# Performance work log

Measured on AMD Instinct MI355X. Metric: run time of the kernel, lower is better.

## Reference

```python
import jax, jax.numpy as jnp
import numpy as np

D_MODEL = 1024
NUM_HEADS = 16
D_K = D_MODEL // NUM_HEADS
NEG = -10000.0


def setup_inputs() -> dict:
    key = jax.random.key(0)
    ks = jax.random.split(key, 8)
    B, S = 2, 2048
    query = jax.random.normal(ks[0], (B, S, D_MODEL), dtype=jnp.float32)
    key_t = jax.random.normal(ks[1], (B, S, D_MODEL), dtype=jnp.float32)
    value = jax.random.normal(ks[2], (B, S, D_MODEL), dtype=jnp.float32)
    mask = jax.random.randint(ks[3], (B, S), 0, 2, dtype=jnp.int32)
    scale = 1.0 / np.sqrt(D_MODEL)
    Wq = jax.random.normal(ks[4], (D_MODEL, D_MODEL), dtype=jnp.float32) * scale
    Wk = jax.random.normal(ks[5], (D_MODEL, D_MODEL), dtype=jnp.float32) * scale
    Wv = jax.random.normal(ks[6], (D_MODEL, D_MODEL), dtype=jnp.float32) * scale
    Wo = jax.random.normal(ks[7], (D_MODEL, D_MODEL), dtype=jnp.float32) * scale
    return {"query": query, "key": key_t, "value": value, "mask": mask,
            "Wq": Wq, "Wk": Wk, "Wv": Wv, "Wo": Wo}


def reference(query, key, value, mask, Wq, Wk, Wv, Wo):
    B, Sq, _ = query.shape
    Sk = key.shape[1]
    # Linear projections (torch Linear: x @ W.T), split heads -> [B,H,S,d_k]
    def proj(x, W, S):
        return (x @ W.T).reshape(B, S, NUM_HEADS, D_K).transpose(0, 2, 1, 3)
    Q = proj(query, Wq, Sq)
    K = proj(key, Wk, Sk)
    V = proj(value, Wv, Sk)
    # scores [B,H,Sq,Sk]
    scores = jnp.einsum("bhqd,bhkd->bhqk", Q, K) / jnp.sqrt(jnp.float32(D_K))
    # padding mask [B,Sk] -> [B,1,1,Sk]
    pad = mask[:, None, None, :]
    scores = jnp.where(pad == 0, NEG, scores)
    # causal mask (mask_future=True)
    causal = jnp.tril(jnp.ones((Sq, Sk), dtype=bool))
    scores = jnp.where(causal, scores, NEG)
    probs = jax.nn.softmax(scores, axis=-1)  # dropout p=0.0 -> identity
    out = jnp.einsum("bhqk,bhkd->bhqd", probs, V)
    out = out.transpose(0, 2, 1, 3).reshape(B, Sq, D_MODEL)
    return out @ Wo.T
```

## Files before the change

### kernel.cpp

```cpp
#include <hip/hip_runtime.h>
#include <hip/hip_bf16.h>

typedef __attribute__((ext_vector_type(8))) short s16x8;
typedef __attribute__((ext_vector_type(4))) float f32x4;

#define MFMA16(a,b,c) __builtin_amdgcn_mfma_f32_16x16x32_bf16((a),(b),(c),0,0,0)

#define GLD16(gp, lp) __builtin_amdgcn_global_load_lds( \
  (const __attribute__((address_space(1))) unsigned int*)(gp), \
  (__attribute__((address_space(3))) unsigned int*)(lp), 16, 0, 0)

static __device__ __forceinline__ unsigned short f2bu(float f) {
  __hip_bfloat16 h = __float2bfloat16(f);
  unsigned short u; __builtin_memcpy(&u, &h, 2); return u;
}
static __device__ __forceinline__ float b2f(unsigned short u) {
  unsigned int x = ((unsigned int)u) << 16; float f; __builtin_memcpy(&f, &x, 4); return f;
}

__global__ __launch_bounds__(256) void cast_all(const float* __restrict__ q, const float* __restrict__ k,
                                                const float* __restrict__ v,
                                                const float* __restrict__ Wq, const float* __restrict__ Wk,
                                                const float* __restrict__ Wv, const float* __restrict__ Wo,
                                                unsigned short* __restrict__ qc, unsigned short* __restrict__ kc,
                                                unsigned short* __restrict__ vc,
                                                unsigned short* __restrict__ wq, unsigned short* __restrict__ wk,
                                                unsigned short* __restrict__ wv, unsigned short* __restrict__ wo) {
  const int y = blockIdx.y;
  const float* in; unsigned short* out; int n4;
  switch (y) {
    case 0: in = q;  out = qc; n4 = 1048576; break;
    case 1: in = k;  out = kc; n4 = 1048576; break;
    case 2: in = v;  out = vc; n4 = 1048576; break;
    case 3: in = Wq; out = wq; n4 = 262144; break;
    case 4: in = Wk; out = wk; n4 = 262144; break;
    case 5: in = Wv; out = wv; n4 = 262144; break;
    default: in = Wo; out = wo; n4 = 262144; break;
  }
  int i = blockIdx.x * 256 + threadIdx.x;
  if (i < n4) {
    float4 val = *(const float4*)(in + (size_t)i * 4);
    unsigned int p0 = (unsigned int)f2bu(val.x) | ((unsigned int)f2bu(val.y) << 16);
    unsigned int p1 = (unsigned int)f2bu(val.z) | ((unsigned int)f2bu(val.w) << 16);
    uint2 pk; pk.x = p0; pk.y = p1;
    *(uint2*)(out + (size_t)i * 4) = pk;
  }
}

static __device__ __forceinline__ void gemm_core(const unsigned short* __restrict__ Aw,
                                                 const unsigned short* __restrict__ Bw,
                                                 int m0, int n0,
                                                 f32x4 (&acc)[4][4],
                                                 unsigned short (*As)[64], unsigned short (*Bs)[64]) {
  const int K = 1024;
  const int tid = threadIdx.x;
  const int lane = tid & 63, wave = tid >> 6;
  const int wm = wave >> 1, wn = wave & 1;
  const int row16 = lane & 15, kgrp = lane >> 4;
  const int srow = lane >> 3, sslot = (lane & 7) ^ srow;
  const int sw = row16 & 7;

  for (int k0 = 0; k0 < K; k0 += 64) {
#pragma unroll
    for (int i = 0; i < 4; i++) {
      int rr = (wave * 4 + i) * 8 + srow;
      GLD16(Aw + (size_t)(m0 + rr) * K + k0 + sslot * 8, (char*)As + (wave * 4 + i) * 1024);
      GLD16(Bw + (size_t)(n0 + rr) * K + k0 + sslot * 8, (char*)Bs + (wave * 4 + i) * 1024);
    }
    __syncthreads();

#pragma unroll
    for (int kk = 0; kk < 2; kk++) {
      s16x8 af[4], bfr[4];
#pragma unroll
      for (int mi = 0; mi < 4; mi++) {
        int rr = wm * 64 + mi * 16 + row16;
        af[mi] = *(const s16x8*)((char*)&As[rr][0] + ((kk * 4 + kgrp) ^ sw) * 16);
      }
#pragma unroll
      for (int ni = 0; ni < 4; ni++) {
        int rr = wn * 64 + ni * 16 + row16;
        bfr[ni] = *(const s16x8*)((char*)&Bs[rr][0] + ((kk * 4 + kgrp) ^ sw) * 16);
      }
#pragma unroll
      for (int mi = 0; mi < 4; mi++)
#pragma unroll
        for (int ni = 0; ni < 4; ni++)
          acc[mi][ni] = MFMA16(af[mi], bfr[ni], acc[mi][ni]);
    }
    __syncthreads();
  }
}

__global__ __launch_bounds__(256) void qkv_gemm(const unsigned short* __restrict__ qc,
                                                const unsigned short* __restrict__ kc,
                                                const unsigned short* __restrict__ vc,
                                                const unsigned short* __restrict__ Wqb,
                                                const unsigned short* __restrict__ Wkb,
                                                const unsigned short* __restrict__ Wvb,
                                                unsigned short* __restrict__ Qb,
                                                unsigned short* __restrict__ Kb,
                                                unsigned short* __restrict__ Vt) {
  __shared__ unsigned short As[128][64];
  __shared__ unsigned short Bs[128][64];
  const int xcd = blockIdx.x & 7, u = blockIdx.x >> 3;
  const int g = xcd * 12 + (u >> 3);
  const int z = g >> 5, mstrip = g & 31;
  const int m0 = mstrip * 128, n0 = (u & 7) * 128;

  const unsigned short* A = (z == 0) ? qc : (z == 1) ? kc : vc;
  const unsigned short* Bw = (z == 0) ? Wqb : (z == 1) ? Wkb : Wvb;

  f32x4 acc[4][4] = {};
  gemm_core(A, Bw, m0, n0, acc, As, Bs);

  const int lane = threadIdx.x & 63, wave = threadIdx.x >> 6;
  const int wm = wave >> 1, wn = wave & 1;
  const int row16 = lane & 15, kgrp = lane >> 4;

  if (z < 2) {
    unsigned short* C = z ? Kb : Qb;
#pragma unroll
    for (int mi = 0; mi < 4; mi++)
#pragma unroll
      for (int ni = 0; ni < 4; ni++)
#pragma unroll
        for (int r = 0; r < 4; r++) {
          int row = m0 + wm * 64 + mi * 16 + kgrp * 4 + r;
          int col = n0 + wn * 64 + ni * 16 + row16;
          C[(size_t)row * 1024 + col] = f2bu(acc[mi][ni][r]);
        }
  } else {
#pragma unroll
    for (int mi = 0; mi < 4; mi++)
#pragma unroll
      for (int ni = 0; ni < 4; ni++) {
        int mb = m0 + wm * 64 + mi * 16 + kgrp * 4;
        int col = n0 + wn * 64 + ni * 16 + row16;
        int bb = mb >> 11, s = mb & 2047;
        unsigned int p0 = (unsigned int)f2bu(acc[mi][ni][0]) | ((unsigned int)f2bu(acc[mi][ni][1]) << 16);
        unsigned int p1 = (unsigned int)f2bu(acc[mi][ni][2]) | ((unsigned int)f2bu(acc[mi][ni][3]) << 16);
        uint2 pk; pk.x = p0; pk.y = p1;
        *(uint2*)&Vt[(((size_t)(bb * 1024 + col)) << 11) + s] = pk;
      }
  }
}

__global__ __launch_bounds__(256) void gemm_wo(const unsigned short* __restrict__ A,
                                               const unsigned short* __restrict__ Bw,
                                               float* __restrict__ C) {
  __shared__ unsigned short As[128][64];
  __shared__ unsigned short Bs[128][64];
  const int xcd = blockIdx.x & 7, u = blockIdx.x >> 3;
  const int g = xcd * 4 + (u >> 3);
  const int m0 = g * 128, n0 = (u & 7) * 128;

  f32x4 acc[4][4] = {};
  gemm_core(A, Bw, m0, n0, acc, As, Bs);

  const int lane = threadIdx.x & 63, wave = threadIdx.x >> 6;
  const int wm = wave >> 1, wn = wave & 1;
  const int row16 = lane & 15, kgrp = lane >> 4;
#pragma unroll
  for (int mi = 0; mi < 4; mi++)
#pragma unroll
    for (int ni = 0; ni < 4; ni++)
#pragma unroll
      for (int r = 0; r < 4; r++) {
        int row = m0 + wm * 64 + mi * 16 + kgrp * 4 + r;
        int col = n0 + wn * 64 + ni * 16 + row16;
        C[(size_t)row * 1024 + col] = acc[mi][ni][r];
      }
}

__global__ __launch_bounds__(256) void fu_kernel(const int* __restrict__ mask, int* __restrict__ fu) {
  const int S = 2048;
  int b = blockIdx.x;
  __shared__ int red[256];
  int best = S;
  for (int k = threadIdx.x; k < S; k += 256)
    if (mask[b * S + k] != 0 && k < best) best = k;
  red[threadIdx.x] = best;
  __syncthreads();
  for (int s = 128; s > 0; s >>= 1) {
    if (threadIdx.x < s) red[threadIdx.x] = min(red[threadIdx.x], red[threadIdx.x + s]);
    __syncthreads();
  }
  if (threadIdx.x == 0) fu[b] = red[0];
}

__global__ __launch_bounds__(256) void reduce_vt(const unsigned short* __restrict__ Vt,
                                                 float* __restrict__ vsum) {
  __shared__ float red[256];
  const unsigned short* p = Vt + ((size_t)blockIdx.x << 11) + threadIdx.x * 8;
  uint4 u = *(const uint4*)p;
  float s = b2f((unsigned short)(u.x & 0xffff));
  s += b2f((unsigned short)(u.x >> 16));
  s += b2f((unsigned short)(u.y & 0xffff));
  s += b2f((unsigned short)(u.y >> 16));
  s += b2f((unsigned short)(u.z & 0xffff));
  s += b2f((unsigned short)(u.z >> 16));
  s += b2f((unsigned short)(u.w & 0xffff));
  s += b2f((unsigned short)(u.w >> 16));
  red[threadIdx.x] = s;
  __syncthreads();
  for (int st = 128; st > 0; st >>= 1) {
    if (threadIdx.x < st) red[threadIdx.x] += red[threadIdx.x + st];
    __syncthreads();
  }
  if (threadIdx.x == 0) vsum[blockIdx.x] = red[0];
}

__global__ __launch_bounds__(256) void flash_attn4(const unsigned short* __restrict__ Q,
                                                   const unsigned short* __restrict__ Kp,
                                                   const unsigned short* __restrict__ Vt,
                                                   const int* __restrict__ mask,
                                                   const int* __restrict__ fu,
                                                   const float* __restrict__ vsum,
                                                   unsigned short* __restrict__ O) {
  const int S = 2048, DM = 1024;
  const int xcd = blockIdx.x & 7, idx = blockIdx.x >> 3;
  const int bh = xcd * 4 + (idx >> 4);
  const int pairq = idx & 15;
  const int b = bh >> 4, h = bh & 15;
  const int tid = threadIdx.x, lane = tid & 63, wave = tid >> 6;
  const int row16 = lane & 15, kgrp = lane >> 4;

  __shared__ unsigned short Ks[2][64][64];
  __shared__ unsigned short Vs[2][64][64];
  __shared__ unsigned short Ps[4][16][72];

  const size_t base = ((size_t)b * S) * DM + h * 64;
  const size_t vtb = ((size_t)(b * 1024 + h * 64)) * S;
  const int* maskb = mask + b * S;

  const int srow = lane >> 3;
  const int sslot = (lane & 7) ^ srow;

  const int fub = fu[b];
  const float* vs = vsum + b * DM + h * 64;
  const int sw = row16 & 7;

#pragma unroll
  for (int pass = 0; pass < 2; ++pass) {
    const int qt = pass ? (31 - pairq) : pairq;
    const int q0 = qt * 64 + wave * 16;
    const int qg = q0 + row16;
    const int nt = qt + 1;

    s16x8 qf0 = *(const s16x8*)&Q[base + (size_t)qg * DM + kgrp * 8];
    s16x8 qf1 = *(const s16x8*)&Q[base + (size_t)qg * DM + 32 + kgrp * 8];

    f32x4 oacc[4] = {};
    float m_run = -1e30f, l_run = 0.f;

    auto stage = [&](int t, int bf) {
      const int kb = t * 64;
#pragma unroll
      for (int c2 = 0; c2 < 2; c2++) {
        const int r = wave * 16 + c2 * 8 + srow;
        GLD16(Kp + base + (size_t)(kb + r) * DM + sslot * 8,
              (char*)&Ks[bf][0][0] + (wave * 2 + c2) * 1024);
        GLD16(Vt + vtb + (size_t)r * S + kb + sslot * 8,
              (char*)&Vs[bf][0][0] + (wave * 2 + c2) * 1024);
      }
    };

    stage(0, 0);
    asm volatile("s_waitcnt vmcnt(0)" ::: "memory");
    __syncthreads();

    int cur = 0;
    for (int t = 0; t < nt; ++t) {
      if (t + 1 < nt) stage(t + 1, cur ^ 1);
      const int kb = t * 64;

      f32x4 sc[4];
#pragma unroll
      for (int nf = 0; nf < 4; nf++) {
        const int rr = nf * 16 + row16;
        s16x8 k0 = *(const s16x8*)&Ks[cur][rr][(kgrp ^ sw) * 8];
        s16x8 k1 = *(const s16x8*)&Ks[cur][rr][((4 + kgrp) ^ sw) * 8];
        f32x4 a = {};
        a = MFMA16(k0, qf0, a);
        a = MFMA16(k1, qf1, a);
        sc[nf] = a;
      }

#pragma unroll
      for (int nf = 0; nf < 4; nf++) {
        const int kbase = kb + nf * 16 + kgrp * 4;
        int4 mv = *(const int4*)&maskb[kbase];
#pragma unroll
        for (int r = 0; r < 4; r++) {
          int m_ok = (r == 0) ? mv.x : (r == 1) ? mv.y : (r == 2) ? mv.z : mv.w;
          float s = sc[nf][r] * 0.125f;
          sc[nf][r] = (kbase + r > qg || m_ok == 0) ? -10000.0f : s;
        }
      }

      float t01 = fmaxf(fmaxf(sc[0][0], sc[0][1]), fmaxf(sc[0][2], sc[0][3]));
      float t23 = fmaxf(fmaxf(sc[1][0], sc[1][1]), fmaxf(sc[1][2], sc[1][3]));
      float t45 = fmaxf(fmaxf(sc[2][0], sc[2][1]), fmaxf(sc[2][2], sc[2][3]));
      float t67 = fmaxf(fmaxf(sc[3][0], sc[3][1]), fmaxf(sc[3][2], sc[3][3]));
      float tmax = fmaxf(fmaxf(t01, t23), fmaxf(t45, t67));
      tmax = fmaxf(tmax, __shfl_xor(tmax, 16));
      tmax = fmaxf(tmax, __shfl_xor(tmax, 32));

      float mnew = fmaxf(m_run, tmax);
      float alpha = __expf(m_run - mnew);
      m_run = mnew;

      float rsum = 0.f;
#pragma unroll
      for (int nf = 0; nf < 4; nf++)
#pragma unroll
        for (int r = 0; r < 4; r++) {
          float p = __expf(sc[nf][r] - mnew);
          sc[nf][r] = p;
          rsum += p;
        }
      rsum += __shfl_xor(rsum, 16);
      rsum += __shfl_xor(rsum, 32);
      l_run = l_run * alpha + rsum;
#pragma unroll
      for (int nf2 = 0; nf2 < 4; nf2++)
#pragma unroll
        for (int r = 0; r < 4; r++) oacc[nf2][r] *= alpha;

#pragma unroll
      for (int nf = 0; nf < 4; nf++) {
        uint2 pk;
        pk.x = (unsigned int)f2bu(sc[nf][0]) | ((unsigned int)f2bu(sc[nf][1]) << 16);
        pk.y = (unsigned int)f2bu(sc[nf][2]) | ((unsigned int)f2bu(sc[nf][3]) << 16);
        *(uint2*)&Ps[wave][row16][nf * 16 + kgrp * 4] = pk;
      }
      s16x8 pf0 = *(const s16x8*)&Ps[wave][row16][kgrp * 8];
      s16x8 pf1 = *(const s16x8*)&Ps[wave][row16][32 + kgrp * 8];

#pragma unroll
      for (int nf2 = 0; nf2 < 4; nf2++) {
        const int rr = nf2 * 16 + row16;
        s16x8 v0 = *(const s16x8*)&Vs[cur][rr][(kgrp ^ sw) * 8];
        s16x8 v1 = *(const s16x8*)&Vs[cur][rr][((4 + kgrp) ^ sw) * 8];
        oacc[nf2] = MFMA16(v0, pf0, oacc[nf2]);
        oacc[nf2] = MFMA16(v1, pf1, oacc[nf2]);
      }

      asm volatile("s_waitcnt vmcnt(0)" ::: "memory");
      __syncthreads();
      cur ^= 1;
    }

    const float rl = 1.0f / l_run;
#pragma unroll
    for (int nf2 = 0; nf2 < 4; nf2++) {
      const int d0 = nf2 * 16 + kgrp * 4;
      float v0 = oacc[nf2][0] * rl, v1 = oacc[nf2][1] * rl;
      float v2 = oacc[nf2][2] * rl, v3 = oacc[nf2][3] * rl;
      if (qg < fub) {
        float4 vv = *(const float4*)&vs[d0];
        v0 = vv.x * (1.0f / 2048.0f);
        v1 = vv.y * (1.0f / 2048.0f);
        v2 = vv.z * (1.0f / 2048.0f);
        v3 = vv.w * (1.0f / 2048.0f);
      }
      uint2 pk;
      pk.x = (unsigned int)f2bu(v0) | ((unsigned int)f2bu(v1) << 16);
      pk.y = (unsigned int)f2bu(v2) | ((unsigned int)f2bu(v3) << 16);
      *(uint2*)&O[base + (size_t)qg * DM + d0] = pk;
    }
  }
}

extern "C" void kernel_launch(void* const* d_in, const int* in_sizes, int n_in,
                              void* d_out, int out_size, void* d_ws, size_t ws_size,
                              hipStream_t stream) {
  const float* q    = (const float*)d_in[0];
  const float* k    = (const float*)d_in[1];
  const float* v    = (const float*)d_in[2];
  const int*   mask = (const int*)d_in[3];
  const float* Wq   = (const float*)d_in[4];
  const float* Wk   = (const float*)d_in[5];
  const float* Wv   = (const float*)d_in[6];
  const float* Wo   = (const float*)d_in[7];
  float* out = (float*)d_out;
  char* ws = (char*)d_ws;

  unsigned short* Wqb  = (unsigned short*)(ws + (size_t)0);
  unsigned short* Wkb  = (unsigned short*)(ws + ((size_t)2 << 20));
  unsigned short* Wvb  = (unsigned short*)(ws + ((size_t)4 << 20));
  unsigned short* Wob  = (unsigned short*)(ws + ((size_t)6 << 20));
  unsigned short* vc   = (unsigned short*)(ws + ((size_t)8 << 20));
  unsigned short* attn = (unsigned short*)(ws + ((size_t)8 << 20));
  unsigned short* Qb   = (unsigned short*)(ws + ((size_t)16 << 20));
  unsigned short* Kb   = (unsigned short*)(ws + ((size_t)24 << 20));
  unsigned short* Vt   = (unsigned short*)(ws + ((size_t)32 << 20));
  float* vsum          = (float*)(ws + ((size_t)40 << 20));
  int*   fub           = (int*)(ws + ((size_t)40 << 20) + (64 << 10));
  unsigned short* qc   = (unsigned short*)d_out;
  unsigned short* kc   = (unsigned short*)d_out + 4194304;

  cast_all<<<dim3(4096, 7), 256, 0, stream>>>(q, k, v, Wq, Wk, Wv, Wo,
                                              qc, kc, vc, Wqb, Wkb, Wvb, Wob);

  qkv_gemm<<<768, 256, 0, stream>>>(qc, kc, vc, Wqb, Wkb, Wvb, Qb, Kb, Vt);

  fu_kernel<<<2, 256, 0, stream>>>(mask, fub);
  reduce_vt<<<2048, 256, 0, stream>>>(Vt, vsum);

  flash_attn4<<<512, 256, 0, stream>>>(Qb, Kb, Vt, mask, fub, vsum, attn);

  gemm_wo<<<256, 256, 0, stream>>>(attn, Wob, out);
}
```

Measured before the change: 151.2 us.

## Split attention into one q-tile per block with additive mask and lazy rescale

The attention kernel no longer pairs two query tiles per block. It launches 1024 blocks, one query tile each, ordered longest-first, and drops the XCD-aware mapping. The padding mask is precomputed as an additive penalty array folded into a single fma with a log2e-prescaled softmax using exp2. The causal compare is applied only on the diagonal tile, and the online-softmax rescale is skipped when no row max increases. This trades per-element ALU work and the paired-tile structure for more blocks and relies on the scheduler to balance the uneven tile lengths. Masked scores now use -30000, which changes the masked value but should not affect the softmax.

New measurement: 144.8 us. 4.2% less time.

```diff
diff --git a/kernel.cpp b/kernel.cpp
--- a/kernel.cpp
+++ b/kernel.cpp
@@ -1,5 +1,6 @@
 #include <hip/hip_runtime.h>
 #include <hip/hip_bf16.h>
+#include <math.h>
 
 typedef __attribute__((ext_vector_type(8))) short s16x8;
 typedef __attribute__((ext_vector_type(4))) float f32x4;
@@ -173,13 +174,17 @@
       }
 }
 
-__global__ __launch_bounds__(256) void fu_kernel(const int* __restrict__ mask, int* __restrict__ fu) {
+__global__ __launch_bounds__(256) void fu_pen_kernel(const int* __restrict__ mask, int* __restrict__ fu,
+                                                     float* __restrict__ pen) {
   const int S = 2048;
   int b = blockIdx.x;
   __shared__ int red[256];
   int best = S;
-  for (int k = threadIdx.x; k < S; k += 256)
-    if (mask[b * S + k] != 0 && k < best) best = k;
+  for (int k = threadIdx.x; k < S; k += 256) {
+    int mv = mask[b * S + k];
+    pen[b * S + k] = mv ? 0.0f : -30000.0f;
+    if (mv != 0 && k < best) best = k;
+  }
   red[threadIdx.x] = best;
   __syncthreads();
   for (int s = 128; s > 0; s >>= 1) {
@@ -211,17 +216,18 @@
   if (threadIdx.x == 0) vsum[blockIdx.x] = red[0];
 }
 
-__global__ __launch_bounds__(256) void flash_attn4(const unsigned short* __restrict__ Q,
+__global__ __launch_bounds__(256) void flash_attn5(const unsigned short* __restrict__ Q,
                                                    const unsigned short* __restrict__ Kp,
                                                    const unsigned short* __restrict__ Vt,
-                                                   const int* __restrict__ mask,
+                                                   const float* __restrict__ pen,
                                                    const int* __restrict__ fu,
                                                    const float* __restrict__ vsum,
                                                    unsigned short* __restrict__ O) {
   const int S = 2048, DM = 1024;
-  const int xcd = blockIdx.x & 7, idx = blockIdx.x >> 3;
-  const int bh = xcd * 4 + (idx >> 4);
-  const int pairq = idx & 15;
+  const float SCALE2 = 0.125f * 1.4426950408889634f;
+  const int bid = blockIdx.x;
+  const int qt = 31 - (bid >> 5);
+  const int bh = bid & 31;
   const int b = bh >> 4, h = bh & 15;
   const int tid = threadIdx.x, lane = tid & 63, wave = tid >> 6;
   const int row16 = lane & 15, kgrp = lane >> 4;
@@ -232,144 +238,152 @@
 
   const size_t base = ((size_t)b * S) * DM + h * 64;
   const size_t vtb = ((size_t)(b * 1024 + h * 64)) * S;
-  const int* maskb = mask + b * S;
+  const float* penb = pen + b * S;
 
   const int srow = lane >> 3;
   const int sslot = (lane & 7) ^ srow;
+  const int sw = row16 & 7;
+
+  const int q0 = qt * 64 + wave * 16;
+  const int qg = q0 + row16;
+  const int nt = qt + 1;
+
+  s16x8 qf0 = *(const s16x8*)&Q[base + (size_t)qg * DM + kgrp * 8];
+  s16x8 qf1 = *(const s16x8*)&Q[base + (size_t)qg * DM + 32 + kgrp * 8];
+
+  f32x4 oacc[4] = {};
+  float m_run = -1e30f, l_run = 0.f;
+
+  auto stage = [&](int t, int bf) {
+    const int kb = t * 64;
+#pragma unroll
+    for (int c2 = 0; c2 < 2; c2++) {
+      const int r = wave * 16 + c2 * 8 + srow;
+      GLD16(Kp + base + (size_t)(kb + r) * DM + sslot * 8,
+            (char*)&Ks[bf][0][0] + (wave * 2 + c2) * 1024);
+      GLD16(Vt + vtb + (size_t)r * S + kb + sslot * 8,
+            (char*)&Vs[bf][0][0] + (wave * 2 + c2) * 1024);
+    }
+  };
+
+  stage(0, 0);
+  asm volatile("s_waitcnt vmcnt(0)" ::: "memory");
+  __syncthreads();
+
+  int cur = 0;
+  for (int t = 0; t < nt; ++t) {
+    if (t + 1 < nt) stage(t + 1, cur ^ 1);
+    const int kb = t * 64;
+
+    float4 pv[4];
+#pragma unroll
+    for (int nf = 0; nf < 4; nf++)
+      pv[nf] = *(const float4*)&penb[kb + nf * 16 + kgrp * 4];
+
+    f32x4 sc[4];
+#pragma unroll
+    for (int nf = 0; nf < 4; nf++) {
+      const int rr = nf * 16 + row16;
+      s16x8 k0 = *(const s16x8*)&Ks[cur][rr][(kgrp ^ sw) * 8];
+      s16x8 k1 = *(const s16x8*)&Ks[cur][rr][((4 + kgrp) ^ sw) * 8];
+      f32x4 a = {};
+      a = MFMA16(k0, qf0, a);
+      a = MFMA16(k1, qf1, a);
+      sc[nf] = a;
+    }
+
+#pragma unroll
+    for (int nf = 0; nf < 4; nf++) {
+      sc[nf][0] = fmaf(sc[nf][0], SCALE2, pv[nf].x);
+      sc[nf][1] = fmaf(sc[nf][1], SCALE2, pv[nf].y);
+      sc[nf][2] = fmaf(sc[nf][2], SCALE2, pv[nf].z);
+      sc[nf][3] = fmaf(sc[nf][3], SCALE2, pv[nf].w);
+    }
+    if (t == nt - 1) {
+#pragma unroll
+      for (int nf = 0; nf < 4; nf++) {
+        const int kbase = kb + nf * 16 + kgrp * 4;
+#pragma unroll
+        for (int r = 0; r < 4; r++)
+          if (kbase + r > qg) sc[nf][r] = -30000.0f;
+      }
+    }
+
+    float t01 = fmaxf(fmaxf(sc[0][0], sc[0][1]), fmaxf(sc[0][2], sc[0][3]));
+    float t23 = fmaxf(fmaxf(sc[1][0], sc[1][1]), fmaxf(sc[1][2], sc[1][3]));
+    float t45 = fmaxf(fmaxf(sc[2][0], sc[2][1]), fmaxf(sc[2][2], sc[2][3]));
+    float t67 = fmaxf(fmaxf(sc[3][0], sc[3][1]), fmaxf(sc[3][2], sc[3][3]));
+    float tmax = fmaxf(fmaxf(t01, t23), fmaxf(t45, t67));
+    tmax = fmaxf(tmax, __shfl_xor(tmax, 16));
+    tmax = fmaxf(tmax, __shfl_xor(tmax, 32));
+
+    if (__any(tmax > m_run)) {
+      float mnew = fmaxf(m_run, tmax);
+      float alpha = __builtin_exp2f(m_run - mnew);
+      m_run = mnew;
+      l_run *= alpha;
+#pragma unroll
+      for (int nf2 = 0; nf2 < 4; nf2++)
+#pragma unroll
+        for (int r = 0; r < 4; r++) oacc[nf2][r] *= alpha;
+    }
+
+    float rsum = 0.f;
+#pragma unroll
+    for (int nf = 0; nf < 4; nf++)
+#pragma unroll
+      for (int r = 0; r < 4; r++) {
+        float p = __builtin_exp2f(sc[nf][r] - m_run);
+        sc[nf][r] = p;
+        rsum += p;
+      }
+    rsum += __shfl_xor(rsum, 16);
+    rsum += __shfl_xor(rsum, 32);
+    l_run += rsum;
+
+#pragma unroll
+    for (int nf = 0; nf < 4; nf++) {
+      uint2 pk;
+      pk.x = (unsigned int)f2bu(sc[nf][0]) | ((unsigned int)f2bu(sc[nf][1]) << 16);
+      pk.y = (unsigned int)f2bu(sc[nf][2]) | ((unsigned int)f2bu(sc[nf][3]) << 16);
+      *(uint2*)&Ps[wave][row16][nf * 16 + kgrp * 4] = pk;
+    }
+    s16x8 pf0 = *(const s16x8*)&Ps[wave][row16][kgrp * 8];
+    s16x8 pf1 = *(const s16x8*)&Ps[wave][row16][32 + kgrp * 8];
+
+#pragma unroll
+    for (int nf2 = 0; nf2 < 4; nf2++) {
+      const int rr = nf2 * 16 + row16;
+      s16x8 v0 = *(const s16x8*)&Vs[cur][rr][(kgrp ^ sw) * 8];
+      s16x8 v1 = *(const s16x8*)&Vs[cur][rr][((4 + kgrp) ^ sw) * 8];
+      oacc[nf2] = MFMA16(v0, pf0, oacc[nf2]);
+      oacc[nf2] = MFMA16(v1, pf1, oacc[nf2]);
+    }
+
+    asm volatile("s_waitcnt vmcnt(0)" ::: "memory");
+    __syncthreads();
+    cur ^= 1;
+  }
 
   const int fub = fu[b];
   const float* vs = vsum + b * DM + h * 64;
-  const int sw = row16 & 7;
-
-#pragma unroll
-  for (int pass = 0; pass < 2; ++pass) {
-    const int qt = pass ? (31 - pairq) : pairq;
-    const int q0 = qt * 64 + wave * 16;
-    const int qg = q0 + row16;
-    const int nt = qt + 1;
-
-    s16x8 qf0 = *(const s16x8*)&Q[base + (size_t)qg * DM + kgrp * 8];
-    s16x8 qf1 = *(const s16x8*)&Q[base + (size_t)qg * DM + 32 + kgrp * 8];
-
-    f32x4 oacc[4] = {};
-    float m_run = -1e30f, l_run = 0.f;
-
-    auto stage = [&](int t, int bf) {
-      const int kb = t * 64;
-#pragma unroll
-      for (int c2 = 0; c2 < 2; c2++) {
-        const int r = wave * 16 + c2 * 8 + srow;
-        GLD16(Kp + base + (size_t)(kb + r) * DM + sslot * 8,
-              (char*)&Ks[bf][0][0] + (wave * 2 + c2) * 1024);
-        GLD16(Vt + vtb + (size_t)r * S + kb + sslot * 8,
-              (char*)&Vs[bf][0][0] + (wave * 2 + c2) * 1024);
-      }
-    };
-
-    stage(0, 0);
-    asm volatile("s_waitcnt vmcnt(0)" ::: "memory");
-    __syncthreads();
-
-    int cur = 0;
-    for (int t = 0; t < nt; ++t) {
-      if (t + 1 < nt) stage(t + 1, cur ^ 1);
-      const int kb = t * 64;
-
-      f32x4 sc[4];
-#pragma unroll
-      for (int nf = 0; nf < 4; nf++) {
-        const int rr = nf * 16 + row16;
-        s16x8 k0 = *(const s16x8*)&Ks[cur][rr][(kgrp ^ sw) * 8];
-        s16x8 k1 = *(const s16x8*)&Ks[cur][rr][((4 + kgrp) ^ sw) * 8];
-        f32x4 a = {};
-        a = MFMA16(k0, qf0, a);
-        a = MFMA16(k1, qf1, a);
-        sc[nf] = a;
-      }
-
-#pragma unroll
-      for (int nf = 0; nf < 4; nf++) {
-        const int kbase = kb + nf * 16 + kgrp * 4;
-        int4 mv = *(const int4*)&maskb[kbase];
-#pragma unroll
-        for (int r = 0; r < 4; r++) {
-          int m_ok = (r == 0) ? mv.x : (r == 1) ? mv.y : (r == 2) ? mv.z : mv.w;
-          float s = sc[nf][r] * 0.125f;
-          sc[nf][r] = (kbase + r > qg || m_ok == 0) ? -10000.0f : s;
-        }
-      }
-
-      float t01 = fmaxf(fmaxf(sc[0][0], sc[0][1]), fmaxf(sc[0][2], sc[0][3]));
-      float t23 = fmaxf(fmaxf(sc[1][0], sc[1][1]), fmaxf(sc[1][2], sc[1][3]));
-      float t45 = fmaxf(fmaxf(sc[2][0], sc[2][1]), fmaxf(sc[2][2], sc[2][3]));
-      float t67 = fmaxf(fmaxf(sc[3][0], sc[3][1]), fmaxf(sc[3][2], sc[3][3]));
-      float tmax = fmaxf(fmaxf(t01, t23), fmaxf(t45, t67));
-      tmax = fmaxf(tmax, __shfl_xor(tmax, 16));
-      tmax = fmaxf(tmax, __shfl_xor(tmax, 32));
-
-      float mnew = fmaxf(m_run, tmax);
-      float alpha = __expf(m_run - mnew);
-      m_run = mnew;
-
-      float rsum = 0.f;
-#pragma unroll
-      for (int nf = 0; nf < 4; nf++)
-#pragma unroll
-        for (int r = 0; r < 4; r++) {
-          float p = __expf(sc[nf][r] - mnew);
-          sc[nf][r] = p;
-          rsum += p;
-        }
-      rsum += __shfl_xor(rsum, 16);
-      rsum += __shfl_xor(rsum, 32);
-      l_run = l_run * alpha + rsum;
-#pragma unroll
-      for (int nf2 = 0; nf2 < 4; nf2++)
-#pragma unroll
-        for (int r = 0; r < 4; r++) oacc[nf2][r] *= alpha;
-
-#pragma unroll
-      for (int nf = 0; nf < 4; nf++) {
-        uint2 pk;
-        pk.x = (unsigned int)f2bu(sc[nf][0]) | ((unsigned int)f2bu(sc[nf][1]) << 16);
-        pk.y = (unsigned int)f2bu(sc[nf][2]) | ((unsigned int)f2bu(sc[nf][3]) << 16);
-        *(uint2*)&Ps[wave][row16][nf * 16 + kgrp * 4] = pk;
-      }
-      s16x8 pf0 = *(const s16x8*)&Ps[wave][row16][kgrp * 8];
-      s16x8 pf1 = *(const s16x8*)&Ps[wave][row16][32 + kgrp * 8];
-
-#pragma unroll
-      for (int nf2 = 0; nf2 < 4; nf2++) {
-        const int rr = nf2 * 16 + row16;
-        s16x8 v0 = *(const s16x8*)&Vs[cur][rr][(kgrp ^ sw) * 8];
-        s16x8 v1 = *(const s16x8*)&Vs[cur][rr][((4 + kgrp) ^ sw) * 8];
-        oacc[nf2] = MFMA16(v0, pf0, oacc[nf2]);
-        oacc[nf2] = MFMA16(v1, pf1, oacc[nf2]);
-      }
-
-      asm volatile("s_waitcnt vmcnt(0)" ::: "memory");
-      __syncthreads();
-      cur ^= 1;
-    }
-
-    const float rl = 1.0f / l_run;
-#pragma unroll
-    for (int nf2 = 0; nf2 < 4; nf2++) {
-      const int d0 = nf2 * 16 + kgrp * 4;
-      float v0 = oacc[nf2][0] * rl, v1 = oacc[nf2][1] * rl;
-      float v2 = oacc[nf2][2] * rl, v3 = oacc[nf2][3] * rl;
-      if (qg < fub) {
-        float4 vv = *(const float4*)&vs[d0];
-        v0 = vv.x * (1.0f / 2048.0f);
-        v1 = vv.y * (1.0f / 2048.0f);
-        v2 = vv.z * (1.0f / 2048.0f);
-        v3 = vv.w * (1.0f / 2048.0f);
-      }
-      uint2 pk;
-      pk.x = (unsigned int)f2bu(v0) | ((unsigned int)f2bu(v1) << 16);
-      pk.y = (unsigned int)f2bu(v2) | ((unsigned int)f2bu(v3) << 16);
-      *(uint2*)&O[base + (size_t)qg * DM + d0] = pk;
-    }
+  const float rl = 1.0f / l_run;
+#pragma unroll
+  for (int nf2 = 0; nf2 < 4; nf2++) {
+    const int d0 = nf2 * 16 + kgrp * 4;
+    float v0 = oacc[nf2][0] * rl, v1 = oacc[nf2][1] * rl;
+    float v2 = oacc[nf2][2] * rl, v3 = oacc[nf2][3] * rl;
+    if (qg < fub) {
+      float4 vv = *(const float4*)&vs[d0];
+      v0 = vv.x * (1.0f / 2048.0f);
+      v1 = vv.y * (1.0f / 2048.0f);
+      v2 = vv.z * (1.0f / 2048.0f);
+      v3 = vv.w * (1.0f / 2048.0f);
+    }
+    uint2 pk;
+    pk.x = (unsigned int)f2bu(v0) | ((unsigned int)f2bu(v1) << 16);
+    pk.y = (unsigned int)f2bu(v2) | ((unsigned int)f2bu(v3) << 16);
+    *(uint2*)&O[base + (size_t)qg * DM + d0] = pk;
   }
 }
 
@@ -398,6 +412,7 @@
   unsigned short* Vt   = (unsigned short*)(ws + ((size_t)32 << 20));
   float* vsum          = (float*)(ws + ((size_t)40 << 20));
   int*   fub           = (int*)(ws + ((size_t)40 << 20) + (64 << 10));
+  float* pen           = (float*)(ws + ((size_t)40 << 20) + (68 << 10));
   unsigned short* qc   = (unsigned short*)d_out;
   unsigned short* kc   = (unsigned short*)d_out + 4194304;
 
@@ -406,10 +421,10 @@
 
   qkv_gemm<<<768, 256, 0, stream>>>(qc, kc, vc, Wqb, Wkb, Wvb, Qb, Kb, Vt);
 
-  fu_kernel<<<2, 256, 0, stream>>>(mask, fub);
+  fu_pen_kernel<<<2, 256, 0, stream>>>(mask, fub, pen);
   reduce_vt<<<2048, 256, 0, stream>>>(Vt, vsum);
 
-  flash_attn4<<<512, 256, 0, stream>>>(Qb, Kb, Vt, mask, fub, vsum, attn);
+  flash_attn5<<<1024, 256, 0, stream>>>(Qb, Kb, Vt, pen, fub, vsum, attn);
 
   gemm_wo<<<256, 256, 0, stream>>>(attn, Wob, out);
 }
```
